# Optimization experiments

Hardware: AMD Instinct MI355X
Metric: run time of the kernel (lower is better)

The kernel has to match this reference:

```python
import jax, jax.numpy as jnp
import numpy as np
from jax import lax

EPS_LN = 1e-5
EPS_NORM = 1e-12

def conv1x1(x, w):
    # x: [b,c,h,w], w: [o,c]
    return jnp.einsum('oc,bchw->bohw', w, x)

def dwconv3x3(x, w):
    # depthwise 3x3, w: [c,1,3,3]
    return lax.conv_general_dilated(
        x, w, window_strides=(1, 1), padding=[(1, 1), (1, 1)],
        feature_group_count=x.shape[1],
        dimension_numbers=('NCHW', 'OIHW', 'NCHW'))

def layernorm_chan(x, w, b):
    # WithBias LayerNorm over channel dim of NCHW (torch does it in b,(hw),c layout)
    mu = jnp.mean(x, axis=1, keepdims=True)
    var = jnp.mean((x - mu) ** 2, axis=1, keepdims=True)
    xn = (x - mu) / jnp.sqrt(var + EPS_LN)
    return xn * w[None, :, None, None] + b[None, :, None, None]

def l2norm(x):
    n = jnp.sqrt(jnp.sum(x * x, axis=-1, keepdims=True))
    return x / jnp.maximum(n, EPS_NORM)

def setup_inputs() -> dict:
    key = jax.random.key(0)
    ks = jax.random.split(key, 8)
    dim, heads, hidden = 64, 2, 170
    b, h, w = 2, 256, 256
    s = 0.05
    return {
        'x': jax.random.normal(ks[0], (b, dim, h, w), jnp.float32),
        'ln1_w': jnp.ones((dim,), jnp.float32),
        'ln1_b': jnp.zeros((dim,), jnp.float32),
        'w_qkv': jax.random.normal(ks[1], (dim * 3, dim), jnp.float32) * s,
        'dw_qkv': jax.random.normal(ks[2], (dim * 3, 1, 3, 3), jnp.float32) * s,
        'temperature': jnp.ones((heads, 1, 1), jnp.float32),
        'w_po': jax.random.normal(ks[3], (dim, dim), jnp.float32) * s,
        'ln2_w': jnp.ones((dim,), jnp.float32),
        'ln2_b': jnp.zeros((dim,), jnp.float32),
        'w_in': jax.random.normal(ks[4], (hidden * 2, dim), jnp.float32) * s,
        'dw_ffn': jax.random.normal(ks[5], (hidden * 2, 1, 3, 3), jnp.float32) * s,
        'w_out': jax.random.normal(ks[6], (dim, hidden), jnp.float32) * s,
    }

def attention(x, w_qkv, dw_qkv, temperature, w_po, num_heads):
    b, c, h, w = x.shape
    qkv = dwconv3x3(conv1x1(x, w_qkv), dw_qkv)            # [b,3c,h,w]
    q, k, v = jnp.split(qkv, 3, axis=1)
    def heads(t):
        return t.reshape(b, num_heads, c // num_heads, h * w)  # [b,hd,ch,hw]
    q, k, v = heads(q), heads(k), heads(v)
    q = l2norm(q)
    k = l2norm(k)
    attn = jnp.einsum('bhcs,bhds->bhcd', q, k) * temperature[None]  # [b,hd,ch,ch]
    attn = jax.nn.softmax(attn, axis=-1)
    out = jnp.einsum('bhcd,bhds->bhcs', attn, v)
    out = out.reshape(b, c, h, w)
    return conv1x1(out, w_po)

def gdfn(x, w_in, dw_ffn, w_out):
    x = dwconv3x3(conv1x1(x, w_in), dw_ffn)
    x1, x2 = jnp.split(x, 2, axis=1)
    return conv1x1(jax.nn.gelu(x1, approximate=False) * x2, w_out)

def reference(x, ln1_w, ln1_b, w_qkv, dw_qkv, temperature, w_po,
              ln2_w, ln2_b, w_in, dw_ffn, w_out):
    num_heads = temperature.shape[0]
    x = x + attention(layernorm_chan(x, ln1_w, ln1_b), w_qkv, dw_qkv,
                      temperature, w_po, num_heads)
    x = x + gdfn(layernorm_chan(x, ln2_w, ln2_b), w_in, dw_ffn, w_out)
    return x
```

## Files before the change

### kernel.cpp

```cpp
#include <hip/hip_runtime.h>
#include <math.h>

#define HW 65536

typedef __attribute__((ext_vector_type(8))) short short8;
typedef __attribute__((ext_vector_type(4))) float floatx4;
typedef __attribute__((ext_vector_type(4))) unsigned short ushortx4;

__device__ __forceinline__ float bf2f(unsigned short u){
  unsigned v = ((unsigned)u)<<16; float f; __builtin_memcpy(&f,&v,4); return f;
}
__device__ __forceinline__ unsigned short f2bf(float f){
  unsigned u; __builtin_memcpy(&u,&f,4);
  u += 0x7fffu + ((u>>16)&1u);
  return (unsigned short)(u>>16);
}
__device__ __forceinline__ int is_f32(const void* magic){
  return ((const unsigned*)magic)[0] == 0x3F800000u;
}
__device__ __forceinline__ float ldv(const void* p, size_t i, int f32){
  return f32 ? ((const float*)p)[i] : bf2f(((const unsigned short*)p)[i]);
}

__global__ __launch_bounds__(64) void k_fold(const void* __restrict__ w_qkv,
                       const void* __restrict__ ln1_w,
                       const void* __restrict__ ln1_b,
                       const void* __restrict__ w_in,
                       const void* __restrict__ ln2_w,
                       const void* __restrict__ ln2_b,
                       const void* __restrict__ w_out,
                       unsigned short* __restrict__ A1, float* __restrict__ a1, float* __restrict__ b1,
                       unsigned short* __restrict__ A5, float* __restrict__ a5, float* __restrict__ b5,
                       unsigned short* __restrict__ A7){
  int f32 = is_f32(ln1_w);
  int bid = blockIdx.x; int c = threadIdx.x;
  if (bid < 192){
    int j = bid;
    float wv = ldv(w_qkv, j*64+c, f32);
    unsigned short q = f2bf(wv*ldv(ln1_w,c,f32));
    A1[j*64+c] = q;
    float sa = bf2f(q);
    float sb = wv*ldv(ln1_b,c,f32);
    #pragma unroll
    for(int o=1;o<64;o<<=1){ sa += __shfl_xor(sa,o,64); sb += __shfl_xor(sb,o,64); }
    if (c==0){ a1[j]=sa; b1[j]=sb; }
  } else if (bid < 576){
    int j = bid-192;
    float wv = (j<340)? ldv(w_in, j*64+c, f32) : 0.f;
    unsigned short q = f2bf(wv*ldv(ln2_w,c,f32));
    A5[j*64+c]=q;
    float sa = bf2f(q);
    float sb = wv*ldv(ln2_b,c,f32);
    #pragma unroll
    for(int o=1;o<64;o<<=1){ sa += __shfl_xor(sa,o,64); sb += __shfl_xor(sb,o,64); }
    if (c==0){ a5[j]=sa; b5[j]=sb; }
  } else {
    int j = bid-576;
    #pragma unroll
    for(int t=0;t<3;t++){
      int k=t*64+c;
      A7[j*192+k] = (k<170)? f2bf(ldv(w_out, j*170+k, f32)) : (unsigned short)0;
    }
  }
}

#define BTT_STR 72
template<int F32>
__device__ __forceinline__ void gemm_ln_body(
    const unsigned short* __restrict__ A, const void* __restrict__ Bv,
    const float* __restrict__ arow, const float* __restrict__ brow,
    unsigned short* __restrict__ out, int outC)
{
  __shared__ unsigned short btt[64*BTT_STR];
  __shared__ float muL[64];
  __shared__ float rsL[64];
  int tid=threadIdx.x; int w=tid>>6, lane=tid&63, m=lane&15, quad=lane>>4;
  int sblk = blockIdx.x*64; int b=sblk>>16, s=sblk&65535;
  int ch = lane, px0 = w*16;
  unsigned short tmp[16];
  {
    size_t src = (size_t)b*64*HW + (size_t)ch*HW + s + px0;
    if (F32){
      const float* sp = (const float*)Bv + src;
      #pragma unroll
      for(int q4=0;q4<4;q4++){
        floatx4 fv = *(const floatx4*)(sp + q4*4);
        #pragma unroll
        for(int k=0;k<4;k++) tmp[q4*4+k] = f2bf(fv[k]);
      }
    } else {
      const unsigned short* sp = (const unsigned short*)Bv + src;
      short8 r0 = *(const short8*)sp;
      short8 r1 = *(const short8*)(sp+8);
      #pragma unroll
      for(int jj=0;jj<8;jj++){ tmp[jj]=(unsigned short)r0[jj]; tmp[8+jj]=(unsigned short)r1[jj]; }
    }
  }
  short8 afA[3][2]; float ajA[3], bjA[3];
  #pragma unroll
  for(int it=0; it<3; it++){
    int j = (w + it*4)*16 + m;
    const unsigned short* ap = A + j*64 + quad*8;
    afA[it][0] = *(const short8*)ap;
    afA[it][1] = *(const short8*)(ap+32);
    ajA[it] = arow[j]; bjA[it] = brow[j];
  }
  #pragma unroll
  for(int jj=0;jj<16;jj++) btt[(px0+jj)*BTT_STR + ch] = tmp[jj];
  __syncthreads();
  short8 bfr[4][2];
  #pragma unroll
  for(int st4=0; st4<4; st4++){
    const unsigned short* row = btt + (st4*16+m)*BTT_STR + quad*8;
    short8 v0 = *(const short8*)row;
    short8 v1 = *(const short8*)(row+32);
    bfr[st4][0]=v0; bfr[st4][1]=v1;
    float sm=0.f, sq=0.f;
    #pragma unroll
    for(int jj=0;jj<8;jj++){
      float a=bf2f((unsigned short)v0[jj]); sm+=a; sq+=a*a;
      float c=bf2f((unsigned short)v1[jj]); sm+=c; sq+=c*c;
    }
    sm += __shfl_xor(sm,16,64); sq += __shfl_xor(sq,16,64);
    sm += __shfl_xor(sm,32,64); sq += __shfl_xor(sq,32,64);
    float m_ = sm*(1.f/64.f);
    float var = sq*(1.f/64.f) - m_*m_;
    if (w==0 && quad==0){ muL[st4*16+m]=m_; rsL[st4*16+m]=1.f/sqrtf(var+1e-5f); }
  }
  __syncthreads();
  floatx4 mh[4], rh[4];
  #pragma unroll
  for(int st4=0; st4<4; st4++){
    mh[st4] = *(const floatx4*)(muL + st4*16 + quad*4);
    rh[st4] = *(const floatx4*)(rsL + st4*16 + quad*4);
  }
  #pragma unroll
  for(int it=0; it<3; it++){
    int j = (w + it*4)*16 + m;
    unsigned short* op = out + ((size_t)b*outC + j)*HW + s;
    #pragma unroll
    for(int st4=0; st4<4; st4++){
      floatx4 acc = {0.f,0.f,0.f,0.f};
      acc = __builtin_amdgcn_mfma_f32_16x16x32_bf16(bfr[st4][0], afA[it][0], acc, 0,0,0);
      acc = __builtin_amdgcn_mfma_f32_16x16x32_bf16(bfr[st4][1], afA[it][1], acc, 0,0,0);
      ushortx4 pk;
      #pragma unroll
      for(int r=0;r<4;r++) pk[r] = f2bf(rh[st4][r]*(acc[r] - mh[st4][r]*ajA[it]) + bjA[it]);
      *(ushortx4*)(op + st4*16 + quad*4) = pk;
    }
  }
}
__global__ __launch_bounds__(256) void k_gemm_ln(
    const unsigned short* __restrict__ A, const void* __restrict__ B,
    const float* __restrict__ arow, const float* __restrict__ brow,
    unsigned short* __restrict__ out,
    int outC, const void* __restrict__ magic, int mode)
{
  int f32 = (mode==1) ? 1 : (mode==2 ? 0 : is_f32(magic));
  if (f32) gemm_ln_body<1>(A,B,arow,brow,out,outC);
  else     gemm_ln_body<0>(A,B,arow,brow,out,outC);
}

#define GTT_STR 200
__global__ __launch_bounds__(256) void k_gemm_out(
    const unsigned short* __restrict__ A7, const unsigned short* __restrict__ G,
    const unsigned short* __restrict__ xmid, void* __restrict__ outp, const void* __restrict__ magic)
{
  __shared__ unsigned short gtt[64*GTT_STR];
  int f32 = is_f32(magic);
  int tid=threadIdx.x; int w=tid>>6, lane=tid&63, m=lane&15, quad=lane>>4;
  int sblk = blockIdx.x*64; int b=sblk>>16, s=sblk&65535;
  const unsigned short* Gb = G + (size_t)b*170*HW + s;
  int px0 = w*16;
  short8 sg0[3], sg1[3];
  #pragma unroll
  for(int rep=0; rep<3; rep++){
    const unsigned short* sp = Gb + (size_t)(rep*64 + lane)*HW + px0;
    sg0[rep] = *(const short8*)sp;
    sg1[rep] = *(const short8*)(sp+8);
  }
  int j = w*16 + m;
  const unsigned short* ap = A7 + j*192 + quad*8;
  short8 af[6];
  #pragma unroll
  for(int ks=0;ks<6;ks++) af[ks] = *(const short8*)(ap + ks*32);
  size_t ibase = ((size_t)b*64 + j)*HW + s + quad*4;
  ushortx4 xm[4];
  #pragma unroll
  for(int st4=0;st4<4;st4++) xm[st4] = *(const ushortx4*)(xmid + ibase + st4*16);
  #pragma unroll
  for(int rep=0; rep<3; rep++){
    int ch = rep*64 + lane;
    #pragma unroll
    for(int jj=0;jj<8;jj++){
      gtt[(px0+jj)*GTT_STR + ch]   = (unsigned short)sg0[rep][jj];
      gtt[(px0+8+jj)*GTT_STR + ch] = (unsigned short)sg1[rep][jj];
    }
  }
  __syncthreads();
  #pragma unroll
  for(int st4=0; st4<4; st4++){
    const unsigned short* row = gtt + (st4*16+m)*GTT_STR + quad*8;
    floatx4 acc = {0.f,0.f,0.f,0.f};
    #pragma unroll
    for(int ks=0;ks<6;ks++){
      short8 bf = *(const short8*)(row + ks*32);
      acc = __builtin_amdgcn_mfma_f32_16x16x32_bf16(bf, af[ks], acc, 0,0,0);
    }
    size_t idx0 = ibase + st4*16;
    if (f32){
      floatx4 o;
      #pragma unroll
      for(int r=0;r<4;r++) o[r] = acc[r] + bf2f(xm[st4][r]);
      *(floatx4*)((float*)outp + idx0) = o;
    } else {
      ushortx4 o;
      #pragma unroll
      for(int r=0;r<4;r++) o[r] = f2bf(acc[r] + bf2f(xm[st4][r]));
      *(ushortx4*)((unsigned short*)outp + idx0) = o;
    }
  }
}

__device__ __forceinline__ void conv_row(const float* __restrict__ r0,
    const float* __restrict__ r1, const float* __restrict__ r2,
    const float* __restrict__ w, float* __restrict__ o){
  #pragma unroll
  for(int k=0;k<8;k++){
    o[k] = w[0]*r0[k] + w[1]*r0[k+1] + w[2]*r0[k+2]
         + w[3]*r1[k] + w[4]*r1[k+1] + w[5]*r1[k+2]
         + w[6]*r2[k] + w[7]*r2[k+1] + w[8]*r2[k+2];
  }
}

#define CVT(F, V) { \
    int lv = __shfl((int)(unsigned short)(V)[7], lane-1, 64); \
    int rv = __shfl((int)(unsigned short)(V)[0], lane+1, 64); \
    F[0] = oct       ? bf2f((unsigned short)lv) : 0.f; \
    F[9] = (oct<31)  ? bf2f((unsigned short)rv) : 0.f; \
    _Pragma("unroll") \
    for(int k=0;k<8;k++) F[k+1] = bf2f((unsigned short)(V)[k]); \
  }

__global__ __launch_bounds__(256,4) void k_dwconv(const unsigned short* __restrict__ src,
    const void* __restrict__ wdw, unsigned short* __restrict__ dst, int C,
    const void* __restrict__ magic){
  int f32 = is_f32(magic);
  int tid=threadIdx.x;
  int bc = blockIdx.y;
  int ch = bc % C;
  int lane = tid&63;
  int oct = tid&31, strip = tid>>5;
  int x0 = oct*8;
  int y0 = blockIdx.x*64 + strip*8;
  const unsigned short* sp = src + (size_t)bc*HW;
  short8 R[10];
  #pragma unroll
  for(int r=0;r<10;r++){
    int y = y0-1+r;
    if((unsigned)y<256u) R[r] = *(const short8*)(sp + y*256 + x0);
    else { short8 z = {0,0,0,0,0,0,0,0}; R[r] = z; }
  }
  float w9[9];
  #pragma unroll
  for(int i=0;i<9;i++) w9[i]=ldv(wdw, ch*9+i, f32);
  unsigned short* dp = dst + (size_t)bc*HW + (size_t)y0*256 + x0;
  float A[10],B[10],C_[10],D[10];
  CVT(A, R[0]) CVT(B, R[1]) CVT(C_, R[2])
#define DSTEP(P,Q,Rr) { \
    float o8[8]; \
    conv_row(P,Q,Rr, w9, o8); \
    short8 st; \
    _Pragma("unroll") \
    for(int k=0;k<8;k++) st[k]=(short)f2bf(o8[k]); \
    *(short8*)dp = st; dp += 256; }
  DSTEP(A,B,C_)  CVT(D, R[3])
  DSTEP(B,C_,D)  CVT(A, R[4])
  DSTEP(C_,D,A)  CVT(B, R[5])
  DSTEP(D,A,B)   CVT(C_,R[6])
  DSTEP(A,B,C_)  CVT(D, R[7])
  DSTEP(B,C_,D)  CVT(A, R[8])
  DSTEP(C_,D,A)  CVT(B, R[9])
  DSTEP(D,A,B)
#undef DSTEP
}

__global__ __launch_bounds__(256) void k_ffn_dw(const unsigned short* __restrict__ src,
    const void* __restrict__ wdw, unsigned short* __restrict__ g,
    const void* __restrict__ magic){
  int f32 = is_f32(magic);
  int tid=threadIdx.x;
  int bi = blockIdx.y;
  int b = bi/170, i = bi - b*170;
  int lane = tid&63;
  int oct = tid&31, strip = tid>>5;
  int x0 = oct*8;
  int y0 = blockIdx.x*64 + strip*8;
  const unsigned short* s1 = src + ((size_t)b*340 + i)*HW;
  const unsigned short* s2 = src + ((size_t)b*340 + 170 + i)*HW;
  short8 R1[10], R2[10];
  #pragma unroll
  for(int r=0;r<10;r++){
    int y = y0-1+r;
    if((unsigned)y<256u){
      int o = y*256 + x0;
      R1[r] = *(const short8*)(s1 + o);
      R2[r] = *(const short8*)(s2 + o);
    } else {
      short8 z = {0,0,0,0,0,0,0,0}; R1[r] = z; R2[r] = z;
    }
  }
  float wa[9], wb[9];
  #pragma unroll
  for(int q=0;q<9;q++){ wa[q]=ldv(wdw, i*9+q, f32); wb[q]=ldv(wdw, (i+170)*9+q, f32); }
  unsigned short* gp = g + ((size_t)b*170 + i)*HW + (size_t)y0*256 + x0;
  float A1[10],B1[10],C1[10],D1[10];
  float A2[10],B2[10],C2[10],D2[10];
  CVT(A1, R1[0]) CVT(B1, R1[1]) CVT(C1, R1[2])
  CVT(A2, R2[0]) CVT(B2, R2[1]) CVT(C2, R2[2])
#define CVT2(S, ri) CVT(S##1, R1[ri]) CVT(S##2, R2[ri])
#define FSTEP(P,Q,Rr) { \
    float oa[8], oc[8]; \
    conv_row(P##1,Q##1,Rr##1, wa, oa); \
    conv_row(P##2,Q##2,Rr##2, wb, oc); \
    short8 st; \
    _Pragma("unroll") \
    for(int k=0;k<8;k++){ \
      float u = oa[k]*(1.59576912f + 0.07135481f*oa[k]*oa[k]); \
      float ge = oa[k]/(1.f + __expf(-u)); \
      st[k]=(short)f2bf(ge*oc[k]); \
    } \
    *(short8*)gp = st; gp += 256; }
  FSTEP(A,B,C)  CVT2(D,3)
  FSTEP(B,C,D)  CVT2(A,4)
  FSTEP(C,D,A)  CVT2(B,5)
  FSTEP(D,A,B)  CVT2(C,6)
  FSTEP(A,B,C)  CVT2(D,7)
  FSTEP(B,C,D)  CVT2(A,8)
  FSTEP(C,D,A)  CVT2(B,9)
  FSTEP(D,A,B)
#undef FSTEP
#undef CVT2
}

__global__ __launch_bounds__(256) void k_attn_qk(const unsigned short* __restrict__ qkv,
    float* __restrict__ S, float* __restrict__ qn, float* __restrict__ kn){
  int tid=threadIdx.x; int w=tid>>6, lane=tid&63, m=lane&15, quad=lane>>4;
  int ct=w>>1, dt=w&1;
  int bh=blockIdx.y; int b=bh>>1, hd=bh&1;
  int p0 = blockIdx.x*512;
  const unsigned short* qrow = qkv + ((size_t)(b*192 + hd*32 + ct*16 + m))*HW + p0 + quad*8;
  const unsigned short* krow = qkv + ((size_t)(b*192 + 64 + hd*32 + dt*16 + m))*HW + p0 + quad*8;
  floatx4 acc = {0.f,0.f,0.f,0.f};
  float nq=0.f, nk=0.f;
  for(int it=0; it<16; it++){
    short8 a = *(const short8*)(qrow + it*32);
    short8 bq = *(const short8*)(krow + it*32);
    if (dt==0){
      #pragma unroll
      for(int jj=0;jj<8;jj++){ float v=bf2f((unsigned short)a[jj]); nq+=v*v; }
    }
    if (ct==0){
      #pragma unroll
      for(int jj=0;jj<8;jj++){ float v=bf2f((unsigned short)bq[jj]); nk+=v*v; }
    }
    acc = __builtin_amdgcn_mfma_f32_16x16x32_bf16(a, bq, acc, 0,0,0);
  }
  nq += __shfl_xor(nq,16,64); nq += __shfl_xor(nq,32,64);
  nk += __shfl_xor(nk,16,64); nk += __shfl_xor(nk,32,64);
  if (dt==0 && quad==0) atomicAdd(&qn[bh*32 + ct*16 + m], nq);
  if (ct==0 && quad==0) atomicAdd(&kn[bh*32 + dt*16 + m], nk);
  #pragma unroll
  for(int r=0;r<4;r++)
    atomicAdd(&S[(bh*32 + ct*16 + quad*4 + r)*32 + dt*16 + m], acc[r]);
}

__global__ void k_attn_fin(const float* __restrict__ S, const float* __restrict__ qn,
    const float* __restrict__ kn, const void* __restrict__ temp,
    const void* __restrict__ w_po, unsigned short* __restrict__ Mbf,
    const void* __restrict__ magic){
  int f32 = is_f32(magic);
  __shared__ float attn[2][32][32];
  __shared__ float invq[64], invk[64];
  int b = blockIdx.x; int tid=threadIdx.x;
  if (tid<64){
    int bh=b*2+(tid>>5); int c=tid&31;
    invq[tid] = 1.f/fmaxf(sqrtf(qn[bh*32+c]),1e-12f);
    invk[tid] = 1.f/fmaxf(sqrtf(kn[bh*32+c]),1e-12f);
  }
  __syncthreads();
  if (tid<64){
    int hd=tid>>5, c=tid&31; int bh=b*2+hd;
    float tmp = ldv(temp, hd, f32);
    float row[32]; float mx=-1e30f;
    for(int d=0;d<32;d++){
      float v = S[(bh*32+c)*32+d]*invq[tid]*invk[hd*32+d]*tmp;
      row[d]=v; mx=fmaxf(mx,v);
    }
    float sum=0.f;
    for(int d=0;d<32;d++){ row[d]=expf(row[d]-mx); sum+=row[d]; }
    float inv=1.f/sum;
    for(int d=0;d<32;d++) attn[hd][c][d]=row[d]*inv;
  }
  __syncthreads();
  for(int idx=tid; idx<4096; idx+=256){
    int o=idx>>6, d=idx&63; int hd=d>>5, dd=d&31;
    float sacc=0.f;
    for(int c=0;c<32;c++) sacc += ldv(w_po, o*64 + hd*32 + c, f32) * attn[hd][c][dd];
    Mbf[(size_t)b*4096 + o*64 + d] = f2bf(sacc);
  }
}

#define XSTR 72
__global__ __launch_bounds__(256) void k_attn_ffn(const void* __restrict__ x,
    const unsigned short* __restrict__ qkv, const unsigned short* __restrict__ Mbf,
    unsigned short* __restrict__ xmid,
    const unsigned short* __restrict__ A5, const float* __restrict__ a5, const float* __restrict__ b5,
    unsigned short* __restrict__ ffn_pre, const void* __restrict__ magic){
  __shared__ unsigned short vtt[64*XSTR];
  __shared__ unsigned short xt[64*XSTR];
  __shared__ float muL[64];
  __shared__ float rsL[64];
  int f32 = is_f32(magic);
  int tid=threadIdx.x; int w=tid>>6, lane=tid&63, m=lane&15, quad=lane>>4;
  int sblk = blockIdx.x*64; int b=sblk>>16, s=sblk&65535;
  int ch = lane, px0 = w*16;
  const unsigned short* vp = qkv + ((size_t)(b*192 + 128))*HW + s + (size_t)ch*HW + px0;
  short8 vr0 = *(const short8*)vp;
  short8 vr1 = *(const short8*)(vp+8);
  int jme = w*16 + m;
  const unsigned short* ap = Mbf + (size_t)b*4096 + jme*64 + quad*8;
  short8 af0 = *(const short8*)ap;
  short8 af1 = *(const short8*)(ap+32);
  size_t xbase = (size_t)b*64*HW + s;
  size_t xi0 = xbase + (size_t)jme*HW + quad*4;
  floatx4 xf[4]; ushortx4 xb[4];
  if (f32){
    #pragma unroll
    for(int st4=0;st4<4;st4++) xf[st4] = *(const floatx4*)((const float*)x + xi0 + st4*16);
  } else {
    #pragma unroll
    for(int st4=0;st4<4;st4++) xb[st4] = *(const ushortx4*)((const unsigned short*)x + xi0 + st4*16);
  }
  short8 gA[6][2]; float aj[6], bj[6];
  #pragma unroll
  for(int it=0; it<3; it++){
    int j = (w + it*4)*16 + m;
    const unsigned short* p5 = A5 + j*64 + quad*8;
    gA[it][0] = *(const short8*)p5;
    gA[it][1] = *(const short8*)(p5+32);
    aj[it] = a5[j]; bj[it] = b5[j];
  }
  #pragma unroll
  for(int jj=0;jj<8;jj++){
    vtt[(px0+jj)*XSTR + ch]   = (unsigned short)vr0[jj];
    vtt[(px0+8+jj)*XSTR + ch] = (unsigned short)vr1[jj];
  }
  __syncthreads();
  short8 bfr[4][2];
  #pragma unroll
  for(int st4=0; st4<4; st4++){
    const unsigned short* row = vtt + (st4*16+m)*XSTR + quad*8;
    bfr[st4][0] = *(const short8*)row;
    bfr[st4][1] = *(const short8*)(row+32);
  }
  #pragma unroll
  for(int st4=0; st4<4; st4++){
    floatx4 acc = {0.f,0.f,0.f,0.f};
    acc = __builtin_amdgcn_mfma_f32_16x16x32_bf16(bfr[st4][0], af0, acc, 0,0,0);
    acc = __builtin_amdgcn_mfma_f32_16x16x32_bf16(bfr[st4][1], af1, acc, 0,0,0);
    size_t idx0 = xi0 + st4*16;
    ushortx4 h;
    if (f32){
      #pragma unroll
      for(int r=0;r<4;r++) h[r] = f2bf(acc[r] + xf[st4][r]);
    } else {
      #pragma unroll
      for(int r=0;r<4;r++) h[r] = f2bf(acc[r] + bf2f(xb[st4][r]));
    }
    *(ushortx4*)(xmid + idx0) = h;
    #pragma unroll
    for(int r=0;r<4;r++) xt[(st4*16+quad*4+r)*XSTR + jme] = h[r];
  }
  __syncthreads();
  #pragma unroll
  for(int st4=0; st4<4; st4++){
    const unsigned short* row = xt + (st4*16+m)*XSTR + quad*8;
    short8 v0 = *(const short8*)row;
    short8 v1 = *(const short8*)(row+32);
    bfr[st4][0]=v0; bfr[st4][1]=v1;
    float sm=0.f, sq=0.f;
    #pragma unroll
    for(int jj=0;jj<8;jj++){
      float a=bf2f((unsigned short)v0[jj]); sm+=a; sq+=a*a;
      float c=bf2f((unsigned short)v1[jj]); sm+=c; sq+=c*c;
    }
    sm += __shfl_xor(sm,16,64); sq += __shfl_xor(sq,16,64);
    sm += __shfl_xor(sm,32,64); sq += __shfl_xor(sq,32,64);
    float m_ = sm*(1.f/64.f);
    float var = sq*(1.f/64.f) - m_*m_;
    if (w==0 && quad==0){ muL[st4*16+m]=m_; rsL[st4*16+m]=1.f/sqrtf(var+1e-5f); }
  }
  __syncthreads();
  floatx4 mh[4], rh[4];
  #pragma unroll
  for(int st4=0; st4<4; st4++){
    mh[st4] = *(const floatx4*)(muL + st4*16 + quad*4);
    rh[st4] = *(const floatx4*)(rsL + st4*16 + quad*4);
  }
  #pragma unroll
  for(int it=0; it<6; it++){
    if (it < 3){
      int jn = (w + (it+3)*4)*16 + m;
      const unsigned short* p5 = A5 + jn*64 + quad*8;
      gA[it+3][0] = *(const short8*)p5;
      gA[it+3][1] = *(const short8*)(p5+32);
      aj[it+3] = a5[jn]; bj[it+3] = b5[jn];
    }
    int j = (w + it*4)*16 + m;
    unsigned short* op = ffn_pre + ((size_t)b*340 + j)*HW + s;
    bool ok = (j < 340);
    #pragma unroll
    for(int st4=0; st4<4; st4++){
      floatx4 acc = {0.f,0.f,0.f,0.f};
      acc = __builtin_amdgcn_mfma_f32_16x16x32_bf16(bfr[st4][0], gA[it][0], acc, 0,0,0);
      acc = __builtin_amdgcn_mfma_f32_16x16x32_bf16(bfr[st4][1], gA[it][1], acc, 0,0,0);
      ushortx4 pk;
      #pragma unroll
      for(int r=0;r<4;r++) pk[r] = f2bf(rh[st4][r]*(acc[r] - mh[st4][r]*aj[it]) + bj[it]);
      if (ok) *(ushortx4*)(op + st4*16 + quad*4) = pk;
    }
  }
}

extern "C" void kernel_launch(void* const* d_in, const int* in_sizes, int n_in,
                              void* d_out, int out_size, void* d_ws, size_t ws_size,
                              hipStream_t stream){
  (void)in_sizes; (void)n_in; (void)out_size; (void)ws_size;
  const void* x     = d_in[0];
  const void* ln1_w = d_in[1];
  const void* ln1_b = d_in[2];
  const void* w_qkv = d_in[3];
  const void* dw_qkv= d_in[4];
  const void* temp  = d_in[5];
  const void* w_po  = d_in[6];
  const void* ln2_w = d_in[7];
  const void* ln2_b = d_in[8];
  const void* w_in  = d_in[9];
  const void* dw_ffn= d_in[10];
  const void* w_out = d_in[11];

  char* ws = (char*)d_ws;
  size_t off = 0;
  auto alloc = [&](size_t n)->void*{ void* p = ws + off; off = (off + n + 255) & ~(size_t)255; return p; };

  unsigned short* A1 = (unsigned short*)alloc(192*64*2);
  float* a1 = (float*)alloc(192*4);
  float* b1 = (float*)alloc(192*4);
  unsigned short* A5 = (unsigned short*)alloc(384*64*2);
  float* a5 = (float*)alloc(384*4);
  float* b5 = (float*)alloc(384*4);
  unsigned short* A7 = (unsigned short*)alloc(64*192*2);
  float* S  = (float*)alloc(4*32*32*4);
  float* qn = (float*)alloc(128*4);
  float* kn = (float*)alloc(128*4);
  unsigned short* Mbf = (unsigned short*)alloc(2*64*64*2);
  unsigned short* xmid = (unsigned short*)alloc((size_t)2*64*HW*2);
  unsigned short* regionA = (unsigned short*)alloc((size_t)2*340*HW*2);
  unsigned short* regionB = (unsigned short*)alloc((size_t)2*192*HW*2);

  k_fold<<<dim3(640), dim3(64), 0, stream>>>(w_qkv, ln1_w, ln1_b, w_in, ln2_w, ln2_b, w_out,
                                             A1, a1, b1, A5, a5, b5, A7);

  k_gemm_ln<<<dim3(2048), dim3(256), 0, stream>>>(A1, x, a1, b1, regionA, 192, ln1_w, 0);
  k_dwconv<<<dim3(4,384), dim3(256), 0, stream>>>(regionA, dw_qkv, regionB, 192, ln1_w);

  hipMemsetAsync(S, 0, 16384+512+512, stream);
  k_attn_qk<<<dim3(128,4), dim3(256), 0, stream>>>(regionB, S, qn, kn);
  k_attn_fin<<<dim3(2), dim3(256), 0, stream>>>(S, qn, kn, temp, w_po, Mbf, ln1_w);

  k_attn_ffn<<<dim3(2048), dim3(256), 0, stream>>>(x, regionB, Mbf, xmid,
                                                   A5, a5, b5, regionA, ln1_w);
  k_ffn_dw<<<dim3(4,340), dim3(256), 0, stream>>>(regionA, dw_ffn, regionB, ln1_w);
  k_gemm_out<<<dim3(2048), dim3(256), 0, stream>>>(A7, regionB, xmid, d_out, ln1_w);
}
```

Baseline: 281.5 us.

## Process four pixel tiles per block with register-prefetched loads in GEMM kernels

Three pointwise GEMM kernels (LN+qkv, attention-out+LN2+ffn-in, ffn-out) now handle four consecutive 64-pixel tiles per block instead of one, launching a quarter as many blocks. Weight fragments are loaded once per block and reused across tiles. The next tile's global loads are issued into registers before the current tile's MFMA and store work, to overlap memory latency with compute. The trade-off is fewer blocks in flight (512 on a large GPU), higher register pressure, and an extra barrier per tile.

```diff
diff --git a/kernel.cpp b/kernel.cpp
--- a/kernel.cpp
+++ b/kernel.cpp
@@ -75,27 +75,8 @@
   __shared__ float muL[64];
   __shared__ float rsL[64];
   int tid=threadIdx.x; int w=tid>>6, lane=tid&63, m=lane&15, quad=lane>>4;
-  int sblk = blockIdx.x*64; int b=sblk>>16, s=sblk&65535;
+  int b = blockIdx.x>>8; int s0 = (blockIdx.x<<8)&65535;
   int ch = lane, px0 = w*16;
-  unsigned short tmp[16];
-  {
-    size_t src = (size_t)b*64*HW + (size_t)ch*HW + s + px0;
-    if (F32){
-      const float* sp = (const float*)Bv + src;
-      #pragma unroll
-      for(int q4=0;q4<4;q4++){
-        floatx4 fv = *(const floatx4*)(sp + q4*4);
-        #pragma unroll
-        for(int k=0;k<4;k++) tmp[q4*4+k] = f2bf(fv[k]);
-      }
-    } else {
-      const unsigned short* sp = (const unsigned short*)Bv + src;
-      short8 r0 = *(const short8*)sp;
-      short8 r1 = *(const short8*)(sp+8);
-      #pragma unroll
-      for(int jj=0;jj<8;jj++){ tmp[jj]=(unsigned short)r0[jj]; tmp[8+jj]=(unsigned short)r1[jj]; }
-    }
-  }
   short8 afA[3][2]; float ajA[3], bjA[3];
   #pragma unroll
   for(int it=0; it<3; it++){
@@ -105,48 +86,81 @@
     afA[it][1] = *(const short8*)(ap+32);
     ajA[it] = arow[j]; bjA[it] = brow[j];
   }
-  #pragma unroll
-  for(int jj=0;jj<16;jj++) btt[(px0+jj)*BTT_STR + ch] = tmp[jj];
-  __syncthreads();
-  short8 bfr[4][2];
-  #pragma unroll
-  for(int st4=0; st4<4; st4++){
-    const unsigned short* row = btt + (st4*16+m)*BTT_STR + quad*8;
-    short8 v0 = *(const short8*)row;
-    short8 v1 = *(const short8*)(row+32);
-    bfr[st4][0]=v0; bfr[st4][1]=v1;
-    float sm=0.f, sq=0.f;
-    #pragma unroll
-    for(int jj=0;jj<8;jj++){
-      float a=bf2f((unsigned short)v0[jj]); sm+=a; sq+=a*a;
-      float c=bf2f((unsigned short)v1[jj]); sm+=c; sq+=c*c;
-    }
-    sm += __shfl_xor(sm,16,64); sq += __shfl_xor(sq,16,64);
-    sm += __shfl_xor(sm,32,64); sq += __shfl_xor(sq,32,64);
-    float m_ = sm*(1.f/64.f);
-    float var = sq*(1.f/64.f) - m_*m_;
-    if (w==0 && quad==0){ muL[st4*16+m]=m_; rsL[st4*16+m]=1.f/sqrtf(var+1e-5f); }
-  }
-  __syncthreads();
-  floatx4 mh[4], rh[4];
-  #pragma unroll
-  for(int st4=0; st4<4; st4++){
-    mh[st4] = *(const floatx4*)(muL + st4*16 + quad*4);
-    rh[st4] = *(const floatx4*)(rsL + st4*16 + quad*4);
-  }
-  #pragma unroll
-  for(int it=0; it<3; it++){
-    int j = (w + it*4)*16 + m;
-    unsigned short* op = out + ((size_t)b*outC + j)*HW + s;
+  size_t sbase = (size_t)b*64*HW + (size_t)ch*HW + px0;
+  floatx4 fr[4]; short8 br0, br1;
+  if (F32){
+    const float* sp = (const float*)Bv + sbase + s0;
+    #pragma unroll
+    for(int q4=0;q4<4;q4++) fr[q4] = *(const floatx4*)(sp + q4*4);
+  } else {
+    const unsigned short* sp = (const unsigned short*)Bv + sbase + s0;
+    br0 = *(const short8*)sp; br1 = *(const short8*)(sp+8);
+  }
+  for(int t=0; t<4; t++){
+    int s = s0 + t*64;
+    unsigned short tmp[16];
+    if (F32){
+      #pragma unroll
+      for(int q4=0;q4<4;q4++)
+        #pragma unroll
+        for(int k=0;k<4;k++) tmp[q4*4+k] = f2bf(fr[q4][k]);
+    } else {
+      #pragma unroll
+      for(int jj=0;jj<8;jj++){ tmp[jj]=(unsigned short)br0[jj]; tmp[8+jj]=(unsigned short)br1[jj]; }
+    }
+    #pragma unroll
+    for(int jj=0;jj<16;jj++) btt[(px0+jj)*BTT_STR + ch] = tmp[jj];
+    __syncthreads();
+    short8 bfr[4][2];
     #pragma unroll
     for(int st4=0; st4<4; st4++){
-      floatx4 acc = {0.f,0.f,0.f,0.f};
-      acc = __builtin_amdgcn_mfma_f32_16x16x32_bf16(bfr[st4][0], afA[it][0], acc, 0,0,0);
-      acc = __builtin_amdgcn_mfma_f32_16x16x32_bf16(bfr[st4][1], afA[it][1], acc, 0,0,0);
-      ushortx4 pk;
-      #pragma unroll
-      for(int r=0;r<4;r++) pk[r] = f2bf(rh[st4][r]*(acc[r] - mh[st4][r]*ajA[it]) + bjA[it]);
-      *(ushortx4*)(op + st4*16 + quad*4) = pk;
+      const unsigned short* row = btt + (st4*16+m)*BTT_STR + quad*8;
+      short8 v0 = *(const short8*)row;
+      short8 v1 = *(const short8*)(row+32);
+      bfr[st4][0]=v0; bfr[st4][1]=v1;
+      float sm=0.f, sq=0.f;
+      #pragma unroll
+      for(int jj=0;jj<8;jj++){
+        float a=bf2f((unsigned short)v0[jj]); sm+=a; sq+=a*a;
+        float c=bf2f((unsigned short)v1[jj]); sm+=c; sq+=c*c;
+      }
+      sm += __shfl_xor(sm,16,64); sq += __shfl_xor(sq,16,64);
+      sm += __shfl_xor(sm,32,64); sq += __shfl_xor(sq,32,64);
+      float m_ = sm*(1.f/64.f);
+      float var = sq*(1.f/64.f) - m_*m_;
+      if (w==0 && quad==0){ muL[st4*16+m]=m_; rsL[st4*16+m]=1.f/sqrtf(var+1e-5f); }
+    }
+    __syncthreads();
+    floatx4 mh[4], rh[4];
+    #pragma unroll
+    for(int st4=0; st4<4; st4++){
+      mh[st4] = *(const floatx4*)(muL + st4*16 + quad*4);
+      rh[st4] = *(const floatx4*)(rsL + st4*16 + quad*4);
+    }
+    if (t<3){
+      if (F32){
+        const float* sp = (const float*)Bv + sbase + s + 64;
+        #pragma unroll
+        for(int q4=0;q4<4;q4++) fr[q4] = *(const floatx4*)(sp + q4*4);
+      } else {
+        const unsigned short* sp = (const unsigned short*)Bv + sbase + s + 64;
+        br0 = *(const short8*)sp; br1 = *(const short8*)(sp+8);
+      }
+    }
+    #pragma unroll
+    for(int it=0; it<3; it++){
+      int j = (w + it*4)*16 + m;
+      unsigned short* op = out + ((size_t)b*outC + j)*HW + s;
+      #pragma unroll
+      for(int st4=0; st4<4; st4++){
+        floatx4 acc = {0.f,0.f,0.f,0.f};
+        acc = __builtin_amdgcn_mfma_f32_16x16x32_bf16(bfr[st4][0], afA[it][0], acc, 0,0,0);
+        acc = __builtin_amdgcn_mfma_f32_16x16x32_bf16(bfr[st4][1], afA[it][1], acc, 0,0,0);
+        ushortx4 pk;
+        #pragma unroll
+        for(int r=0;r<4;r++) pk[r] = f2bf(rh[st4][r]*(acc[r] - mh[st4][r]*ajA[it]) + bjA[it]);
+        *(ushortx4*)(op + st4*16 + quad*4) = pk;
+      }
     }
   }
 }
@@ -169,55 +183,75 @@
   __shared__ unsigned short gtt[64*GTT_STR];
   int f32 = is_f32(magic);
   int tid=threadIdx.x; int w=tid>>6, lane=tid&63, m=lane&15, quad=lane>>4;
-  int sblk = blockIdx.x*64; int b=sblk>>16, s=sblk&65535;
-  const unsigned short* Gb = G + (size_t)b*170*HW + s;
+  int b = blockIdx.x>>8; int s0 = (blockIdx.x<<8)&65535;
   int px0 = w*16;
-  short8 sg0[3], sg1[3];
-  #pragma unroll
-  for(int rep=0; rep<3; rep++){
-    const unsigned short* sp = Gb + (size_t)(rep*64 + lane)*HW + px0;
-    sg0[rep] = *(const short8*)sp;
-    sg1[rep] = *(const short8*)(sp+8);
-  }
   int j = w*16 + m;
   const unsigned short* ap = A7 + j*192 + quad*8;
   short8 af[6];
   #pragma unroll
   for(int ks=0;ks<6;ks++) af[ks] = *(const short8*)(ap + ks*32);
-  size_t ibase = ((size_t)b*64 + j)*HW + s + quad*4;
-  ushortx4 xm[4];
-  #pragma unroll
-  for(int st4=0;st4<4;st4++) xm[st4] = *(const ushortx4*)(xmid + ibase + st4*16);
+  const unsigned short* Gb = G + (size_t)b*170*HW + px0;
+  size_t ib = ((size_t)b*64 + j)*HW + quad*4;
+  short8 sg0[3], sg1[3]; ushortx4 xm[4];
   #pragma unroll
   for(int rep=0; rep<3; rep++){
-    int ch = rep*64 + lane;
-    #pragma unroll
-    for(int jj=0;jj<8;jj++){
-      gtt[(px0+jj)*GTT_STR + ch]   = (unsigned short)sg0[rep][jj];
-      gtt[(px0+8+jj)*GTT_STR + ch] = (unsigned short)sg1[rep][jj];
-    }
-  }
-  __syncthreads();
-  #pragma unroll
-  for(int st4=0; st4<4; st4++){
-    const unsigned short* row = gtt + (st4*16+m)*GTT_STR + quad*8;
-    floatx4 acc = {0.f,0.f,0.f,0.f};
-    #pragma unroll
-    for(int ks=0;ks<6;ks++){
-      short8 bf = *(const short8*)(row + ks*32);
-      acc = __builtin_amdgcn_mfma_f32_16x16x32_bf16(bf, af[ks], acc, 0,0,0);
-    }
-    size_t idx0 = ibase + st4*16;
-    if (f32){
-      floatx4 o;
-      #pragma unroll
-      for(int r=0;r<4;r++) o[r] = acc[r] + bf2f(xm[st4][r]);
-      *(floatx4*)((float*)outp + idx0) = o;
-    } else {
-      ushortx4 o;
-      #pragma unroll
-      for(int r=0;r<4;r++) o[r] = f2bf(acc[r] + bf2f(xm[st4][r]));
-      *(ushortx4*)((unsigned short*)outp + idx0) = o;
+    const unsigned short* sp = Gb + (size_t)(rep*64 + lane)*HW + s0;
+    sg0[rep] = *(const short8*)sp;
+    sg1[rep] = *(const short8*)(sp+8);
+  }
+  #pragma unroll
+  for(int st4=0;st4<4;st4++) xm[st4] = *(const ushortx4*)(xmid + ib + s0 + st4*16);
+  for(int t=0; t<4; t++){
+    int s = s0 + t*64;
+    #pragma unroll
+    for(int rep=0; rep<3; rep++){
+      int ch = rep*64 + lane;
+      #pragma unroll
+      for(int jj=0;jj<8;jj++){
+        gtt[(px0+jj)*GTT_STR + ch]   = (unsigned short)sg0[rep][jj];
+        gtt[(px0+8+jj)*GTT_STR + ch] = (unsigned short)sg1[rep][jj];
+      }
+    }
+    __syncthreads();
+    short8 sn0[3], sn1[3]; ushortx4 xn[4];
+    if (t<3){
+      #pragma unroll
+      for(int rep=0; rep<3; rep++){
+        const unsigned short* sp = Gb + (size_t)(rep*64 + lane)*HW + s + 64;
+        sn0[rep] = *(const short8*)sp;
+        sn1[rep] = *(const short8*)(sp+8);
+      }
+      #pragma unroll
+      for(int st4=0;st4<4;st4++) xn[st4] = *(const ushortx4*)(xmid + ib + s + 64 + st4*16);
+    }
+    #pragma unroll
+    for(int st4=0; st4<4; st4++){
+      const unsigned short* row = gtt + (st4*16+m)*GTT_STR + quad*8;
+      floatx4 acc = {0.f,0.f,0.f,0.f};
+      #pragma unroll
+      for(int ks=0;ks<6;ks++){
+        short8 bf = *(const short8*)(row + ks*32);
+        acc = __builtin_amdgcn_mfma_f32_16x16x32_bf16(bf, af[ks], acc, 0,0,0);
+      }
+      size_t idx0 = ib + s + st4*16;
+      if (f32){
+        floatx4 o;
+        #pragma unroll
+        for(int r=0;r<4;r++) o[r] = acc[r] + bf2f(xm[st4][r]);
+        *(floatx4*)((float*)outp + idx0) = o;
+      } else {
+        ushortx4 o;
+        #pragma unroll
+        for(int r=0;r<4;r++) o[r] = f2bf(acc[r] + bf2f(xm[st4][r]));
+        *(ushortx4*)((unsigned short*)outp + idx0) = o;
+      }
+    }
+    __syncthreads();
+    if (t<3){
+      #pragma unroll
+      for(int rep=0;rep<3;rep++){ sg0[rep]=sn0[rep]; sg1[rep]=sn1[rep]; }
+      #pragma unroll
+      for(int st4=0;st4<4;st4++) xm[st4]=xn[st4];
     }
   }
 }
@@ -423,112 +457,122 @@
   __shared__ float rsL[64];
   int f32 = is_f32(magic);
   int tid=threadIdx.x; int w=tid>>6, lane=tid&63, m=lane&15, quad=lane>>4;
-  int sblk = blockIdx.x*64; int b=sblk>>16, s=sblk&65535;
+  int b = blockIdx.x>>8; int s0 = (blockIdx.x<<8)&65535;
   int ch = lane, px0 = w*16;
-  const unsigned short* vp = qkv + ((size_t)(b*192 + 128))*HW + s + (size_t)ch*HW + px0;
-  short8 vr0 = *(const short8*)vp;
-  short8 vr1 = *(const short8*)(vp+8);
   int jme = w*16 + m;
   const unsigned short* ap = Mbf + (size_t)b*4096 + jme*64 + quad*8;
   short8 af0 = *(const short8*)ap;
   short8 af1 = *(const short8*)(ap+32);
-  size_t xbase = (size_t)b*64*HW + s;
-  size_t xi0 = xbase + (size_t)jme*HW + quad*4;
-  floatx4 xf[4]; ushortx4 xb[4];
-  if (f32){
-    #pragma unroll
-    for(int st4=0;st4<4;st4++) xf[st4] = *(const floatx4*)((const float*)x + xi0 + st4*16);
-  } else {
-    #pragma unroll
-    for(int st4=0;st4<4;st4++) xb[st4] = *(const ushortx4*)((const unsigned short*)x + xi0 + st4*16);
-  }
   short8 gA[6][2]; float aj[6], bj[6];
   #pragma unroll
-  for(int it=0; it<3; it++){
+  for(int it=0; it<6; it++){
     int j = (w + it*4)*16 + m;
     const unsigned short* p5 = A5 + j*64 + quad*8;
     gA[it][0] = *(const short8*)p5;
     gA[it][1] = *(const short8*)(p5+32);
     aj[it] = a5[j]; bj[it] = b5[j];
   }
-  #pragma unroll
-  for(int jj=0;jj<8;jj++){
-    vtt[(px0+jj)*XSTR + ch]   = (unsigned short)vr0[jj];
-    vtt[(px0+8+jj)*XSTR + ch] = (unsigned short)vr1[jj];
-  }
-  __syncthreads();
-  short8 bfr[4][2];
-  #pragma unroll
-  for(int st4=0; st4<4; st4++){
-    const unsigned short* row = vtt + (st4*16+m)*XSTR + quad*8;
-    bfr[st4][0] = *(const short8*)row;
-    bfr[st4][1] = *(const short8*)(row+32);
-  }
-  #pragma unroll
-  for(int st4=0; st4<4; st4++){
-    floatx4 acc = {0.f,0.f,0.f,0.f};
-    acc = __builtin_amdgcn_mfma_f32_16x16x32_bf16(bfr[st4][0], af0, acc, 0,0,0);
-    acc = __builtin_amdgcn_mfma_f32_16x16x32_bf16(bfr[st4][1], af1, acc, 0,0,0);
-    size_t idx0 = xi0 + st4*16;
-    ushortx4 h;
-    if (f32){
-      #pragma unroll
-      for(int r=0;r<4;r++) h[r] = f2bf(acc[r] + xf[st4][r]);
-    } else {
-      #pragma unroll
-      for(int r=0;r<4;r++) h[r] = f2bf(acc[r] + bf2f(xb[st4][r]));
-    }
-    *(ushortx4*)(xmid + idx0) = h;
-    #pragma unroll
-    for(int r=0;r<4;r++) xt[(st4*16+quad*4+r)*XSTR + jme] = h[r];
-  }
-  __syncthreads();
-  #pragma unroll
-  for(int st4=0; st4<4; st4++){
-    const unsigned short* row = xt + (st4*16+m)*XSTR + quad*8;
-    short8 v0 = *(const short8*)row;
-    short8 v1 = *(const short8*)(row+32);
-    bfr[st4][0]=v0; bfr[st4][1]=v1;
-    float sm=0.f, sq=0.f;
+  const unsigned short* vbase = qkv + ((size_t)(b*192 + 128) + ch)*HW + px0;
+  size_t xrow = ((size_t)b*64 + jme)*HW + quad*4;
+  short8 vr0 = *(const short8*)(vbase + s0);
+  short8 vr1 = *(const short8*)(vbase + s0 + 8);
+  floatx4 xf[4]; ushortx4 xb[4];
+  if (f32){
+    const float* xp = (const float*)x + xrow + s0;
+    #pragma unroll
+    for(int st4=0;st4<4;st4++) xf[st4] = *(const floatx4*)(xp + st4*16);
+  } else {
+    const unsigned short* xp = (const unsigned short*)x + xrow + s0;
+    #pragma unroll
+    for(int st4=0;st4<4;st4++) xb[st4] = *(const ushortx4*)(xp + st4*16);
+  }
+  for(int t=0; t<4; t++){
+    int s = s0 + t*64;
     #pragma unroll
     for(int jj=0;jj<8;jj++){
-      float a=bf2f((unsigned short)v0[jj]); sm+=a; sq+=a*a;
-      float c=bf2f((unsigned short)v1[jj]); sm+=c; sq+=c*c;
-    }
-    sm += __shfl_xor(sm,16,64); sq += __shfl_xor(sq,16,64);
-    sm += __shfl_xor(sm,32,64); sq += __shfl_xor(sq,32,64);
-    float m_ = sm*(1.f/64.f);
-    float var = sq*(1.f/64.f) - m_*m_;
-    if (w==0 && quad==0){ muL[st4*16+m]=m_; rsL[st4*16+m]=1.f/sqrtf(var+1e-5f); }
-  }
-  __syncthreads();
-  floatx4 mh[4], rh[4];
-  #pragma unroll
-  for(int st4=0; st4<4; st4++){
-    mh[st4] = *(const floatx4*)(muL + st4*16 + quad*4);
-    rh[st4] = *(const floatx4*)(rsL + st4*16 + quad*4);
-  }
-  #pragma unroll
-  for(int it=0; it<6; it++){
-    if (it < 3){
-      int jn = (w + (it+3)*4)*16 + m;
-      const unsigned short* p5 = A5 + jn*64 + quad*8;
-      gA[it+3][0] = *(const short8*)p5;
-      gA[it+3][1] = *(const short8*)(p5+32);
-      aj[it+3] = a5[jn]; bj[it+3] = b5[jn];
-    }
-    int j = (w + it*4)*16 + m;
-    unsigned short* op = ffn_pre + ((size_t)b*340 + j)*HW + s;
-    bool ok = (j < 340);
+      vtt[(px0+jj)*XSTR + ch]   = (unsigned short)vr0[jj];
+      vtt[(px0+8+jj)*XSTR + ch] = (unsigned short)vr1[jj];
+    }
+    __syncthreads();
+    short8 bfr[4][2];
+    #pragma unroll
+    for(int st4=0; st4<4; st4++){
+      const unsigned short* row = vtt + (st4*16+m)*XSTR + quad*8;
+      bfr[st4][0] = *(const short8*)row;
+      bfr[st4][1] = *(const short8*)(row+32);
+    }
     #pragma unroll
     for(int st4=0; st4<4; st4++){
       floatx4 acc = {0.f,0.f,0.f,0.f};
-      acc = __builtin_amdgcn_mfma_f32_16x16x32_bf16(bfr[st4][0], gA[it][0], acc, 0,0,0);
-      acc = __builtin_amdgcn_mfma_f32_16x16x32_bf16(bfr[st4][1], gA[it][1], acc, 0,0,0);
-      ushortx4 pk;
-      #pragma unroll
-      for(int r=0;r<4;r++) pk[r] = f2bf(rh[st4][r]*(acc[r] - mh[st4][r]*aj[it]) + bj[it]);
-      if (ok) *(ushortx4*)(op + st4*16 + quad*4) = pk;
+      acc = __builtin_amdgcn_mfma_f32_16x16x32_bf16(bfr[st4][0], af0, acc, 0,0,0);
+      acc = __builtin_amdgcn_mfma_f32_16x16x32_bf16(bfr[st4][1], af1, acc, 0,0,0);
+      size_t idx0 = xrow + s + st4*16;
+      ushortx4 h;
+      if (f32){
+        #pragma unroll
+        for(int r=0;r<4;r++) h[r] = f2bf(acc[r] + xf[st4][r]);
+      } else {
+        #pragma unroll
+        for(int r=0;r<4;r++) h[r] = f2bf(acc[r] + bf2f(xb[st4][r]));
+      }
+      *(ushortx4*)(xmid + idx0) = h;
+      #pragma unroll
+      for(int r=0;r<4;r++) xt[(st4*16+quad*4+r)*XSTR + jme] = h[r];
+    }
+    __syncthreads();
+    #pragma unroll
+    for(int st4=0; st4<4; st4++){
+      const unsigned short* row = xt + (st4*16+m)*XSTR + quad*8;
+      short8 v0 = *(const short8*)row;
+      short8 v1 = *(const short8*)(row+32);
+      bfr[st4][0]=v0; bfr[st4][1]=v1;
+      float sm=0.f, sq=0.f;
+      #pragma unroll
+      for(int jj=0;jj<8;jj++){
+        float a=bf2f((unsigned short)v0[jj]); sm+=a; sq+=a*a;
+        float c=bf2f((unsigned short)v1[jj]); sm+=c; sq+=c*c;
+      }
+      sm += __shfl_xor(sm,16,64); sq += __shfl_xor(sq,16,64);
+      sm += __shfl_xor(sm,32,64); sq += __shfl_xor(sq,32,64);
+      float m_ = sm*(1.f/64.f);
+      float var = sq*(1.f/64.f) - m_*m_;
+      if (w==0 && quad==0){ muL[st4*16+m]=m_; rsL[st4*16+m]=1.f/sqrtf(var+1e-5f); }
+    }
+    __syncthreads();
+    floatx4 mh[4], rh[4];
+    #pragma unroll
+    for(int st4=0; st4<4; st4++){
+      mh[st4] = *(const floatx4*)(muL + st4*16 + quad*4);
+      rh[st4] = *(const floatx4*)(rsL + st4*16 + quad*4);
+    }
+    if (t<3){
+      vr0 = *(const short8*)(vbase + s + 64);
+      vr1 = *(const short8*)(vbase + s + 64 + 8);
+      if (f32){
+        const float* xp = (const float*)x + xrow + s + 64;
+        #pragma unroll
+        for(int st4=0;st4<4;st4++) xf[st4] = *(const floatx4*)(xp + st4*16);
+      } else {
+        const unsigned short* xp = (const unsigned short*)x + xrow + s + 64;
+        #pragma unroll
+        for(int st4=0;st4<4;st4++) xb[st4] = *(const ushortx4*)(xp + st4*16);
+      }
+    }
+    #pragma unroll
+    for(int it=0; it<6; it++){
+      int j = (w + it*4)*16 + m;
+      unsigned short* op = ffn_pre + ((size_t)b*340 + j)*HW + s;
+      bool ok = (j < 340);
+      #pragma unroll
+      for(int st4=0; st4<4; st4++){
+        floatx4 acc = {0.f,0.f,0.f,0.f};
+        acc = __builtin_amdgcn_mfma_f32_16x16x32_bf16(bfr[st4][0], gA[it][0], acc, 0,0,0);
+        acc = __builtin_amdgcn_mfma_f32_16x16x32_bf16(bfr[st4][1], gA[it][1], acc, 0,0,0);
+        ushortx4 pk;
+        #pragma unroll
+        for(int r=0;r<4;r++) pk[r] = f2bf(rh[st4][r]*(acc[r] - mh[st4][r]*aj[it]) + bj[it]);
+        if (ok) *(ushortx4*)(op + st4*16 + quad*4) = pk;
+      }
     }
   }
 }
@@ -572,15 +616,15 @@
   k_fold<<<dim3(640), dim3(64), 0, stream>>>(w_qkv, ln1_w, ln1_b, w_in, ln2_w, ln2_b, w_out,
                                              A1, a1, b1, A5, a5, b5, A7);
 
-  k_gemm_ln<<<dim3(2048), dim3(256), 0, stream>>>(A1, x, a1, b1, regionA, 192, ln1_w, 0);
+  k_gemm_ln<<<dim3(512), dim3(256), 0, stream>>>(A1, x, a1, b1, regionA, 192, ln1_w, 0);
   k_dwconv<<<dim3(4,384), dim3(256), 0, stream>>>(regionA, dw_qkv, regionB, 192, ln1_w);
 
   hipMemsetAsync(S, 0, 16384+512+512, stream);
   k_attn_qk<<<dim3(128,4), dim3(256), 0, stream>>>(regionB, S, qn, kn);
   k_attn_fin<<<dim3(2), dim3(256), 0, stream>>>(S, qn, kn, temp, w_po, Mbf, ln1_w);
 
-  k_attn_ffn<<<dim3(2048), dim3(256), 0, stream>>>(x, regionB, Mbf, xmid,
-                                                   A5, a5, b5, regionA, ln1_w);
+  k_attn_ffn<<<dim3(512), dim3(256), 0, stream>>>(x, regionB, Mbf, xmid,
+                                                  A5, a5, b5, regionA, ln1_w);
   k_ffn_dw<<<dim3(4,340), dim3(256), 0, stream>>>(regionA, dw_ffn, regionB, ln1_w);
-  k_gemm_out<<<dim3(2048), dim3(256), 0, stream>>>(A7, regionB, xmid, d_out, ln1_w);
-}
+  k_gemm_out<<<dim3(512), dim3(256), 0, stream>>>(A7, regionB, xmid, d_out, ln1_w);
+}
```

Result: no change. 277.7 us, median of 2 (-1.3%).
